# Kernel optimization log

Hardware: AMD Instinct MI355X
Metric: run time of the kernel (lower is better)

Reference implementation:

```python
import jax, jax.numpy as jnp
import numpy as np

D = 1024        # d_model
H = 16          # n_heads
DF = 4096       # d_ff
MAXL = 1024     # max_len
MAXSTEPS = 24   # max_steps


def setup_inputs() -> dict:
    key = jax.random.key(0)
    ks = jax.random.split(key, 10)
    B, S = 4, 1024
    s = 0.02
    f32 = jnp.float32
    return {
        "x": jax.random.normal(ks[0], (B, S, D), f32),
        "original_input": jax.random.normal(ks[1], (B, S, D), f32),
        "think_step": 5,
        "step_embed": jax.random.normal(ks[2], (MAXSTEPS, D), f32) * s,
        "Wqkv": jax.random.normal(ks[3], (D, 3 * D), f32) * s,
        "bqkv": jnp.zeros((3 * D,), f32),
        "Wout": jax.random.normal(ks[4], (D, D), f32) * s,
        "bout": jnp.zeros((D,), f32),
        "Wg": jax.random.normal(ks[5], (2 * D, D), f32) * s,
        "bg": jnp.zeros((D,), f32),
        "rel_pos_bias": jax.random.normal(ks[6], (2 * MAXL - 1,), f32) * s,
        "W1": jax.random.normal(ks[7], (D, DF), f32) * s,
        "b1": jnp.zeros((DF,), f32),
        "W2": jax.random.normal(ks[8], (DF, D), f32) * s,
        "b2": jnp.zeros((D,), f32),
        "ln1_g": jnp.ones((D,), f32),
        "ln1_b": jnp.zeros((D,), f32),
        "ln2_g": jnp.ones((D,), f32),
        "ln2_b": jnp.zeros((D,), f32),
    }


def _layer_norm(x, g, b, eps=1e-5):
    m = jnp.mean(x, axis=-1, keepdims=True)
    v = jnp.mean((x - m) ** 2, axis=-1, keepdims=True)
    return (x - m) * jax.lax.rsqrt(v + eps) * g + b


def reference(x, original_input, think_step, step_embed, Wqkv, bqkv, Wout, bout,
              Wg, bg, rel_pos_bias, W1, b1, W2, b2, ln1_g, ln1_b, ln2_g, ln2_b):
    B, S, _ = x.shape
    hd = D // H
    # gated residual input injection
    gate = jax.nn.sigmoid(jnp.concatenate([x, original_input], axis=-1) @ Wg + bg)
    x = x * (1.0 - gate) + original_input * gate
    # think-step embedding (clamped)
    step = min(int(think_step), MAXSTEPS - 1)
    x = x + step_embed[step][None, None, :]
    # qkv projection -> (3, B, H, S, hd)
    qkv = (x @ Wqkv + bqkv).reshape(B, S, 3, H, hd).transpose(2, 0, 3, 1, 4)
    q, k, v = qkv[0], qkv[1], qkv[2]
    scores = jnp.einsum('bhqd,bhkd->bhqk', q, k) * (hd ** -0.5)
    # relative position bias: dist clamped to [0, 2*MAXL-2]
    pos = jnp.arange(S)
    rel = jnp.clip(pos[:, None] - pos[None, :] + (MAXL - 1), 0, 2 * MAXL - 2)
    scores = scores + rel_pos_bias[rel][None, None]  # (B,H,S,S)
    probs = jax.nn.softmax(scores, axis=-1)
    attn = jnp.einsum('bhqk,bhkd->bhqd', probs, v)
    attn = attn.transpose(0, 2, 1, 3).reshape(B, S, D)
    attn = attn @ Wout + bout
    x = _layer_norm(x + attn, ln1_g, ln1_b)
    h = jax.nn.gelu(x @ W1 + b1, approximate=False) @ W2 + b2
    return _layer_norm(x + h, ln2_g, ln2_b)
```

## Files before the change

kernel.cpp:

```cpp
#include <hip/hip_runtime.h>
#include <hip/hip_bf16.h>
#include <math.h>

#define D_MODEL 1024
#define NH      16
#define HD      64
#define DFF     4096
#define SEQ     1024
#define BATCH   4
#define TOK     (BATCH*SEQ)
#define MAXSTEPS 24

typedef __hip_bfloat16 bf16;
typedef __attribute__((ext_vector_type(8))) short short8;
typedef __attribute__((ext_vector_type(4))) float floatx4;

__device__ __forceinline__ float b2f(bf16 v){ return __bfloat162float(v); }
__device__ __forceinline__ bf16  f2b(float v){ return __float2bfloat16(v); }

__device__ __forceinline__ void gload_lds16(const bf16* g, bf16* l){
    __builtin_amdgcn_global_load_lds((const __attribute__((address_space(1))) void*)g,
                                     (__attribute__((address_space(3))) void*)l, 16, 0, 0);
}

template<int TN, int EPI, bool SPLITK>
__global__ __launch_bounds__(256)
void mfma_gemm(const bf16* __restrict__ A, const bf16* __restrict__ Bt,
               const float* __restrict__ bias, void* __restrict__ outv,
               void* __restrict__ outv2,
               int M, int N, int K, int lda, int ldb,
               const float* __restrict__ xg, const float* __restrict__ og,
               const float* __restrict__ seg, const int* __restrict__ stepp)
{
    constexpr int NT  = TN / 32;
    constexpr int NBP = TN / 64;
    constexpr int R   = (TN == 64) ? 4 : 3;
    __shared__ bf16 As[R][128 * 32];
    __shared__ bf16 Bs[R][TN * 32];
    const int tid  = threadIdx.x;
    const int lane = tid & 63;
    const int w    = tid >> 6;
    const int wm   = w & 1, wn = w >> 1;
    const int fr   = lane & 15;
    const int q    = lane >> 4;

    if (SPLITK) {
        int z = blockIdx.z;
        A  += (size_t)z * K;
        Bt += (size_t)z * K;
    }

    const int tn_g = gridDim.x;
    const int nwg  = tn_g * gridDim.y;
    const int bid  = blockIdx.y * tn_g + blockIdx.x;
    const int o    = (bid & 7) * (nwg >> 3) + (bid >> 3);
    const int bandw = 8 * tn_g;
    const int band  = o / bandw;
    const int rr    = o - band * bandw;
    const int row0 = (band * 8 + (rr & 7)) * 128;
    const int col0 = (rr >> 3) * TN;

    const bf16* gA[2]; int sA_[2];
    #pragma unroll
    for (int p = 0; p < 2; ++p) {
        int s  = p * 256 + tid;
        int m  = s >> 2;
        int qg = (s & 3) ^ ((m >> 1) & 3);
        gA[p]  = A + (size_t)(row0 + m) * lda + qg * 8;
        sA_[p] = s * 8;
    }
    const bf16* gB[NBP]; int sB_[NBP];
    #pragma unroll
    for (int p = 0; p < NBP; ++p) {
        int s  = p * 256 + tid;
        int m  = s >> 2;
        int qg = (s & 3) ^ ((m >> 1) & 3);
        gB[p]  = Bt + (size_t)(col0 + m) * ldb + qg * 8;
        sB_[p] = s * 8;
    }

    int aoff[4], boff[NT];
    #pragma unroll
    for (int t = 0; t < 4; ++t) {
        int ml  = wm * 64 + t * 16 + fr;
        aoff[t] = (ml * 4 + (q ^ ((ml >> 1) & 3))) * 8;
    }
    #pragma unroll
    for (int t = 0; t < NT; ++t) {
        int nl  = wn * (TN / 2) + t * 16 + fr;
        boff[t] = (nl * 4 + (q ^ ((nl >> 1) & 3))) * 8;
    }

    #pragma unroll
    for (int pt = 0; pt < R - 1; ++pt) {
        #pragma unroll
        for (int p = 0; p < 2; ++p)   gload_lds16(gA[p] + pt * 32, &As[pt][sA_[p]]);
        #pragma unroll
        for (int p = 0; p < NBP; ++p) gload_lds16(gB[p] + pt * 32, &Bs[pt][sB_[p]]);
    }

    floatx4 acc[4][NT] = {};
    const int nk = K >> 5;
    int cur = 0;
    int kst = (R - 1) * 32;

    for (int t = 0; t < nk; ++t) {
        if constexpr (TN == 64) asm volatile("s_waitcnt vmcnt(6)" ::: "memory");
        else                    asm volatile("s_waitcnt vmcnt(4)" ::: "memory");
        __builtin_amdgcn_s_barrier();
        asm volatile("" ::: "memory");

        if (kst < K) {
            int sb = (cur == 0) ? (R - 1) : (cur - 1);
            #pragma unroll
            for (int p = 0; p < 2; ++p)   gload_lds16(gA[p] + kst, &As[sb][sA_[p]]);
            #pragma unroll
            for (int p = 0; p < NBP; ++p) gload_lds16(gB[p] + kst, &Bs[sb][sB_[p]]);
            kst += 32;
        }

        short8 af[4], bfg[NT];
        #pragma unroll
        for (int i = 0; i < 4; ++i)  af[i]  = *(const short8*)(&As[cur][aoff[i]]);
        #pragma unroll
        for (int j = 0; j < NT; ++j) bfg[j] = *(const short8*)(&Bs[cur][boff[j]]);
        #pragma unroll
        for (int i = 0; i < 4; ++i)
            #pragma unroll
            for (int j = 0; j < NT; ++j)
                acc[i][j] = __builtin_amdgcn_mfma_f32_16x16x32_bf16(af[i], bfg[j], acc[i][j], 0, 0, 0);

        cur = (cur == R - 1) ? 0 : (cur + 1);
    }

    void* outp = outv;
    float bscale = 1.0f;
    if (SPLITK && blockIdx.z != 0) { outp = outv2; bscale = 0.0f; }

    int st = 0;
    if (EPI == 3) {
        st = stepp[0];
        st = st < 0 ? 0 : (st > MAXSTEPS - 1 ? MAXSTEPS - 1 : st);
    }

    float bv[NT], sv[NT];
    #pragma unroll
    for (int nt = 0; nt < NT; ++nt) {
        int col = col0 + wn * (TN / 2) + nt * 16 + fr;
        bv[nt] = bias[col] * bscale;
        if (EPI == 3) sv[nt] = seg[st * D_MODEL + col];
    }
    #pragma unroll
    for (int mt = 0; mt < 4; ++mt) {
        #pragma unroll
        for (int nt = 0; nt < NT; ++nt) {
            int col = col0 + wn * (TN / 2) + nt * 16 + fr;
            #pragma unroll
            for (int r = 0; r < 4; ++r) {
                int row = row0 + wm * 64 + mt * 16 + q * 4 + r;
                float v = acc[mt][nt][r] + bv[nt];
                if (EPI == 0) {
                    ((float*)outp)[(size_t)row * N + col] = v;
                } else if (EPI == 1) {
                    ((bf16*)outp)[(size_t)row * N + col] = f2b(v);
                } else if (EPI == 2) {
                    float g = 0.5f * v * (1.0f + erff(v * 0.70710678118654752f));
                    ((bf16*)outp)[(size_t)row * N + col] = f2b(g);
                } else if (EPI == 3) {
                    float g = 1.0f / (1.0f + __expf(-v));
                    size_t idx = (size_t)row * N + col;
                    float mix = xg[idx] * (1.0f - g) + og[idx] * g + sv[nt];
                    ((bf16*)outp)[idx] = f2b(mix);
                } else {
                    if (col0 < 2048) {
                        ((bf16*)outp)[(size_t)row * N + col] = f2b(v);
                    } else {
                        int b = row >> 10, s = row & 1023;
                        int hh = (col - 2048) >> 6, d = (col - 2048) & 63;
                        ((bf16*)outv2)[((size_t)((b * NH + hh) * 64 + d)) * SEQ + s] = f2b(v);
                    }
                }
            }
        }
    }
}

__global__ __launch_bounds__(256, 2)
void gemm_wide_gelu(const bf16* __restrict__ A, const bf16* __restrict__ Bt,
                    const float* __restrict__ bias, bf16* __restrict__ out,
                    int M, int N, int K)
{
    constexpr int R = 3;
    __shared__ bf16 As[R][256 * 32];
    __shared__ bf16 Bs[R][128 * 32];
    const int tid  = threadIdx.x;
    const int lane = tid & 63;
    const int w    = tid >> 6;
    const int wm   = w & 1, wn = w >> 1;
    const int fr   = lane & 15;
    const int q    = lane >> 4;

    const int tn_g = gridDim.x;
    const int nwg  = tn_g * gridDim.y;
    const int bid  = blockIdx.y * tn_g + blockIdx.x;
    const int o    = (bid & 7) * (nwg >> 3) + (bid >> 3);
    const int bandw = 8 * tn_g;
    const int band  = o / bandw;
    const int rr    = o - band * bandw;
    const int row0 = (band * 8 + (rr & 7)) * 256;
    const int col0 = (rr >> 3) * 128;

    const bf16* gA[4]; int sA_[4];
    #pragma unroll
    for (int p = 0; p < 4; ++p) {
        int s  = p * 256 + tid;
        int m  = s >> 2;
        int qg = (s & 3) ^ ((m >> 1) & 3);
        gA[p]  = A + (size_t)(row0 + m) * K + qg * 8;
        sA_[p] = s * 8;
    }
    const bf16* gB[2]; int sB_[2];
    #pragma unroll
    for (int p = 0; p < 2; ++p) {
        int s  = p * 256 + tid;
        int m  = s >> 2;
        int qg = (s & 3) ^ ((m >> 1) & 3);
        gB[p]  = Bt + (size_t)(col0 + m) * K + qg * 8;
        sB_[p] = s * 8;
    }

    int aoff[8], boff[4];
    #pragma unroll
    for (int t = 0; t < 8; ++t) {
        int ml  = wm * 128 + t * 16 + fr;
        aoff[t] = (ml * 4 + (q ^ ((ml >> 1) & 3))) * 8;
    }
    #pragma unroll
    for (int t = 0; t < 4; ++t) {
        int nl  = wn * 64 + t * 16 + fr;
        boff[t] = (nl * 4 + (q ^ ((nl >> 1) & 3))) * 8;
    }

    #pragma unroll
    for (int pt = 0; pt < R - 1; ++pt) {
        #pragma unroll
        for (int p = 0; p < 4; ++p) gload_lds16(gA[p] + pt * 32, &As[pt][sA_[p]]);
        #pragma unroll
        for (int p = 0; p < 2; ++p) gload_lds16(gB[p] + pt * 32, &Bs[pt][sB_[p]]);
    }

    floatx4 acc[8][4] = {};
    const int nk = K >> 5;
    int cur = 0;
    int kst = (R - 1) * 32;

    for (int t = 0; t < nk; ++t) {
        asm volatile("s_waitcnt vmcnt(6)" ::: "memory");
        __builtin_amdgcn_s_barrier();
        asm volatile("" ::: "memory");

        if (kst < K) {
            int sb = (cur == 0) ? (R - 1) : (cur - 1);
            #pragma unroll
            for (int p = 0; p < 4; ++p) gload_lds16(gA[p] + kst, &As[sb][sA_[p]]);
            #pragma unroll
            for (int p = 0; p < 2; ++p) gload_lds16(gB[p] + kst, &Bs[sb][sB_[p]]);
            kst += 32;
        }

        short8 af[8], bfg[4];
        #pragma unroll
        for (int i = 0; i < 8; ++i) af[i]  = *(const short8*)(&As[cur][aoff[i]]);
        #pragma unroll
        for (int j = 0; j < 4; ++j) bfg[j] = *(const short8*)(&Bs[cur][boff[j]]);
        __builtin_amdgcn_s_setprio(1);
        #pragma unroll
        for (int i = 0; i < 8; ++i)
            #pragma unroll
            for (int j = 0; j < 4; ++j)
                acc[i][j] = __builtin_amdgcn_mfma_f32_16x16x32_bf16(af[i], bfg[j], acc[i][j], 0, 0, 0);
        __builtin_amdgcn_s_setprio(0);

        cur = (cur == R - 1) ? 0 : (cur + 1);
    }

    float bv[4];
    #pragma unroll
    for (int j = 0; j < 4; ++j) bv[j] = bias[col0 + wn * 64 + j * 16 + fr];
    #pragma unroll
    for (int mt = 0; mt < 8; ++mt) {
        #pragma unroll
        for (int nt = 0; nt < 4; ++nt) {
            int col = col0 + wn * 64 + nt * 16 + fr;
            #pragma unroll
            for (int r = 0; r < 4; ++r) {
                int row = row0 + wm * 128 + mt * 16 + q * 4 + r;
                float v = acc[mt][nt][r] + bv[nt];
                float g = 0.5f * v * (1.0f + erff(v * 0.70710678118654752f));
                out[(size_t)row * N + col] = f2b(g);
            }
        }
    }
}

#define NTRANS_BLOCKS 14336
__global__ __launch_bounds__(256)
void transpose_all_kernel(const float* __restrict__ Wg,   bf16* __restrict__ WgT,
                          const float* __restrict__ Wqkv, bf16* __restrict__ WqkvT,
                          const float* __restrict__ Wout, bf16* __restrict__ WoutT,
                          const float* __restrict__ W1,   bf16* __restrict__ W1T,
                          const float* __restrict__ W2,   bf16* __restrict__ W2T)
{
    __shared__ float t[32][33];
    const int bid = blockIdx.x;
    if (bid >= NTRANS_BLOCKS) return;
    const float* W; bf16* WT; int K, N, base;
    if      (bid <  2048) { W = Wg;   WT = WgT;   K = 2048; N = 1024; base = 0; }
    else if (bid <  5120) { W = Wqkv; WT = WqkvT; K = 1024; N = 3072; base = 2048; }
    else if (bid <  6144) { W = Wout; WT = WoutT; K = 1024; N = 1024; base = 5120; }
    else if (bid < 10240) { W = W1;   WT = W1T;   K = 1024; N = 4096; base = 6144; }
    else                  { W = W2;   WT = W2T;   K = 4096; N = 1024; base = 10240; }
    const int lb  = bid - base;
    const int ntx = N >> 5;
    const int n0 = (lb % ntx) * 32, k0 = (lb / ntx) * 32;
    const int tx = threadIdx.x & 31, ty = threadIdx.x >> 5;
    #pragma unroll
    for (int i = 0; i < 4; ++i)
        t[ty + i * 8][tx] = W[(size_t)(k0 + ty + i * 8) * N + n0 + tx];
    __syncthreads();
    #pragma unroll
    for (int i = 0; i < 4; ++i)
        WT[(size_t)(n0 + ty + i * 8) * K + k0 + tx] = f2b(t[tx][ty + i * 8]);
}

__global__ __launch_bounds__(256)
void xcat_kernel(const float* __restrict__ x, const float* __restrict__ orig,
                 bf16* __restrict__ xcat)
{
    int i = blockIdx.x * 256 + threadIdx.x;
    float4 xv = ((const float4*)x)[i];
    float4 ov = ((const float4*)orig)[i];
    int t = i >> 8, c4 = (i & 255) * 4;
    bf16* px = xcat + (size_t)t * 2048 + c4;
    px[0] = f2b(xv.x); px[1] = f2b(xv.y); px[2] = f2b(xv.z); px[3] = f2b(xv.w);
    bf16* po = px + 1024;
    po[0] = f2b(ov.x); po[1] = f2b(ov.y); po[2] = f2b(ov.z); po[3] = f2b(ov.w);
}

__global__ __launch_bounds__(256)
void fattn_kernel(const bf16* __restrict__ qkv, const bf16* __restrict__ Vt,
                  const float* __restrict__ relb, bf16* __restrict__ out)
{
    __shared__ bf16 KPs[128 * 64];
    __shared__ bf16 Vs [64 * 128];
    __shared__ float relb_s[1088];

    const int tid  = threadIdx.x;
    const int lane = tid & 63;
    const int w    = tid >> 6;
    const int fr   = lane & 15;
    const int quad = lane >> 4;

    const int qt = blockIdx.x & 15;
    const int h  = (blockIdx.x >> 4) & 15;
    const int b  = blockIdx.x >> 8;
    const int bq = b * SEQ;
    const int bh = b * NH + h;

    for (int i = tid; i < 1087; i += 256)
        relb_s[i] = relb[qt * 64 + i] - 8.0f;

    const int qrow = bq + qt * 64 + w * 16 + fr;
    short8 qf[2];
    {
        const bf16* qp = qkv + (size_t)qrow * 3072 + h * 64 + quad * 8;
        qf[0] = *(const short8*)(qp);
        qf[1] = *(const short8*)(qp + 32);
    }

    int ibase[4];
    #pragma unroll
    for (int r = 0; r < 4; ++r)
        ibase[r] = (w * 16 + quad * 4 + r) - fr + 1023;

    float lsum[4] = {0.f, 0.f, 0.f, 0.f};
    floatx4 accO[4];
    #pragma unroll
    for (int nt = 0; nt < 4; ++nt) accO[nt] = (floatx4){0.f, 0.f, 0.f, 0.f};

    for (int k0 = 0; k0 < SEQ; k0 += 128) {
        __syncthreads();
        #pragma unroll
        for (int it = 0; it < 4; ++it) {
            int s = it * 256 + tid;
            int key = s >> 3, cs = s & 7;
            int c = cs ^ (key & 7);
            const bf16* src = qkv + (size_t)(bq + k0 + key) * 3072 + 1024 + h * 64 + c * 8;
            gload_lds16(src, KPs + (size_t)s * 8);
        }
        #pragma unroll
        for (int it = 0; it < 4; ++it) {
            int s = it * 256 + tid;
            int row = s >> 4, cs = s & 15;
            int c = cs ^ (row & 15);
            const bf16* src = Vt + (size_t)(bh * 64 + row) * SEQ + k0 + c * 8;
            gload_lds16(src, Vs + (size_t)s * 8);
        }
        __syncthreads();

        floatx4 accS[8];
        #pragma unroll
        for (int t = 0; t < 8; ++t) accS[t] = (floatx4){0.f, 0.f, 0.f, 0.f};
        __builtin_amdgcn_s_setprio(1);
        #pragma unroll
        for (int t = 0; t < 8; ++t) {
            int row = t * 16 + fr;
            #pragma unroll
            for (int ks = 0; ks < 2; ++ks) {
                int slot = (ks * 4 + quad) ^ (row & 7);
                short8 kf = *(const short8*)(KPs + (size_t)row * 64 + slot * 8);
                accS[t] = __builtin_amdgcn_mfma_f32_16x16x32_bf16(qf[ks], kf, accS[t], 0, 0, 0);
            }
        }
        __builtin_amdgcn_s_setprio(0);

        __syncthreads();

        bf16* Ps = KPs + w * 2048;
        #pragma unroll
        for (int t = 0; t < 8; ++t) {
            int keyl = t * 16 + fr;
            int cbase = keyl >> 3, koff = keyl & 7;
            #pragma unroll
            for (int r = 0; r < 4; ++r) {
                float bias = relb_s[ibase[r] - k0 - t * 16];
                float p = __expf(fmaf(accS[t][r], 0.125f, bias));
                lsum[r] += p;
                int row = quad * 4 + r;
                int slot = cbase ^ (row & 15);
                Ps[(size_t)row * 128 + slot * 8 + koff] = f2b(p);
            }
        }

        __builtin_amdgcn_s_setprio(1);
        #pragma unroll
        for (int ks = 0; ks < 4; ++ks) {
            int slotp = (ks * 4 + quad) ^ (fr & 15);
            short8 pf = *(const short8*)(Ps + (size_t)fr * 128 + slotp * 8);
            #pragma unroll
            for (int nt = 0; nt < 4; ++nt) {
                int vrow = nt * 16 + fr;
                int slotv = (ks * 4 + quad) ^ (vrow & 15);
                short8 vf = *(const short8*)(Vs + (size_t)vrow * 128 + slotv * 8);
                accO[nt] = __builtin_amdgcn_mfma_f32_16x16x32_bf16(pf, vf, accO[nt], 0, 0, 0);
            }
        }
        __builtin_amdgcn_s_setprio(0);
    }

    float inv[4];
    #pragma unroll
    for (int r = 0; r < 4; ++r) {
        float v = lsum[r];
        v += __shfl_xor(v, 1); v += __shfl_xor(v, 2);
        v += __shfl_xor(v, 4); v += __shfl_xor(v, 8);
        inv[r] = 1.0f / v;
    }

    #pragma unroll
    for (int nt = 0; nt < 4; ++nt) {
        int col = h * 64 + nt * 16 + fr;
        #pragma unroll
        for (int r = 0; r < 4; ++r) {
            int t = bq + qt * 64 + w * 16 + quad * 4 + r;
            out[(size_t)t * D_MODEL + col] = f2b(accO[nt][r] * inv[r]);
        }
    }
}

template<bool OUT_BF16, bool HAS2>
__global__ __launch_bounds__(256)
void ln_kernel(const bf16* __restrict__ a, const float* __restrict__ add,
               const float* __restrict__ add2,
               const float* __restrict__ g, const float* __restrict__ bb,
               void* __restrict__ outv)
{
    __shared__ float red[256];
    __shared__ float red2[256];
    const int row = blockIdx.x;
    const int tid = threadIdx.x;
    float s[4];
    float lsum = 0.f, lsq = 0.f;
    #pragma unroll
    for (int u = 0; u < 4; ++u) {
        int i = tid + 256 * u;
        float v = b2f(a[row * D_MODEL + i]) + add[row * D_MODEL + i];
        if (HAS2) v += add2[row * D_MODEL + i];
        s[u] = v; lsum += v; lsq += v * v;
    }
    red[tid] = lsum; red2[tid] = lsq; __syncthreads();
    for (int s2 = 128; s2 > 0; s2 >>= 1) {
        if (tid < s2) { red[tid] += red[tid + s2]; red2[tid] += red2[tid + s2]; }
        __syncthreads();
    }
    float mean = red[0] * (1.0f / D_MODEL);
    float var  = red2[0] * (1.0f / D_MODEL) - mean * mean;
    float rs = rsqrtf(var + 1e-5f);
    #pragma unroll
    for (int u = 0; u < 4; ++u) {
        int i = tid + 256 * u;
        float o = (s[u] - mean) * rs * g[i] + bb[i];
        if (OUT_BF16) ((bf16*)outv)[row * D_MODEL + i] = f2b(o);
        else          ((float*)outv)[row * D_MODEL + i] = o;
    }
}

extern "C" void kernel_launch(void* const* d_in, const int* in_sizes, int n_in,
                              void* d_out, int out_size, void* d_ws, size_t ws_size,
                              hipStream_t stream)
{
    const float* x     = (const float*)d_in[0];
    const float* orig  = (const float*)d_in[1];
    const int*   step  = (const int*)  d_in[2];
    const float* se    = (const float*)d_in[3];
    const float* Wqkv  = (const float*)d_in[4];
    const float* bqkv  = (const float*)d_in[5];
    const float* Wout  = (const float*)d_in[6];
    const float* bout  = (const float*)d_in[7];
    const float* Wg    = (const float*)d_in[8];
    const float* bg    = (const float*)d_in[9];
    const float* relb  = (const float*)d_in[10];
    const float* W1    = (const float*)d_in[11];
    const float* b1    = (const float*)d_in[12];
    const float* W2    = (const float*)d_in[13];
    const float* b2    = (const float*)d_in[14];
    const float* ln1g  = (const float*)d_in[15];
    const float* ln1b  = (const float*)d_in[16];
    const float* ln2g  = (const float*)d_in[17];
    const float* ln2b  = (const float*)d_in[18];

    char* ws = (char*)d_ws;
    bf16* WgT   = (bf16*)(ws);
    bf16* WqkvT = (bf16*)(ws + ( 4u << 20));
    bf16* WoutT = (bf16*)(ws + (10u << 20));
    bf16* W1T   = (bf16*)(ws + (12u << 20));
    bf16* W2T   = (bf16*)(ws + (20u << 20));
    bf16* xw    = (bf16*)(ws + (28u << 20));
    bf16* xcat  = (bf16*)(ws + (36u << 20));
    bf16* attnb = (bf16*)(ws + (36u << 20));
    bf16* h     = (bf16*)(ws + (44u << 20));
    bf16* qkvb  = (bf16*)(ws + (52u << 20));
    float* tmp2 = (float*)(ws);
    bf16* Vt    = (bf16*)d_out;
    float* tmp  = (float*)d_out;

    dim3 blk(256);

    transpose_all_kernel<<<NTRANS_BLOCKS, blk, 0, stream>>>(Wg, WgT, Wqkv, WqkvT,
                                                    Wout, WoutT, W1, W1T, W2, W2T);
    xcat_kernel<<<TOK, blk, 0, stream>>>(x, orig, xcat);

    mfma_gemm<64, 3, false><<<dim3(D_MODEL/64, TOK/128), blk, 0, stream>>>(
        xcat, WgT, bg, xw, nullptr, TOK, D_MODEL, 2*D_MODEL, 2*D_MODEL, 2*D_MODEL,
        x, orig, se, step);

    mfma_gemm<128, 4, false><<<dim3(3*D_MODEL/128, TOK/128), blk, 0, stream>>>(
        xw, WqkvT, bqkv, qkvb, Vt, TOK, 3*D_MODEL, D_MODEL, D_MODEL, D_MODEL,
        nullptr, nullptr, nullptr, nullptr);

    fattn_kernel<<<BATCH*NH*(SEQ/64), blk, 0, stream>>>(qkvb, Vt, relb, attnb);

    mfma_gemm<64, 0, false><<<dim3(D_MODEL/64, TOK/128), blk, 0, stream>>>(
        attnb, WoutT, bout, tmp, nullptr, TOK, D_MODEL, D_MODEL, D_MODEL, D_MODEL,
        nullptr, nullptr, nullptr, nullptr);

    ln_kernel<true, false><<<TOK, blk, 0, stream>>>(xw, tmp, nullptr, ln1g, ln1b, xw);

    gemm_wide_gelu<<<dim3(DFF/128, TOK/256), blk, 0, stream>>>(
        xw, W1T, b1, h, TOK, DFF, D_MODEL);

    mfma_gemm<128, 0, true><<<dim3(D_MODEL/128, TOK/128, 2), blk, 0, stream>>>(
        h, W2T, b2, tmp, tmp2, TOK, D_MODEL, DFF/2, DFF, DFF,
        nullptr, nullptr, nullptr, nullptr);

    ln_kernel<false, true><<<TOK, blk, 0, stream>>>(xw, tmp, tmp2, ln2g, ln2b, d_out);
}
```

Baseline: 429.5 us.

## Fuse fp32-to-bf16 cast into gate GEMM, use wide GEMM for QKV

Adds a gate GEMM that reads x and original_input in fp32 directly, converts them to bf16 while staging into LDS, and runs the sigmoid-mix epilogue, so the separate concat/cast kernel and its buffer are gone. The QKV projection moves to the 256-row wide GEMM template with a plain bf16 epilogue. A separate transpose kernel then builds the V layout for attention, where the old scattered transposed-store epilogue used to do it. The gate GEMM trades async LDS loads of A for register-staged conversion with only double buffering, and the extra transpose adds a launch plus another pass over V.

```diff
diff --git a/kernel.cpp b/kernel.cpp
--- a/kernel.cpp
+++ b/kernel.cpp
@@ -28,9 +28,7 @@
 void mfma_gemm(const bf16* __restrict__ A, const bf16* __restrict__ Bt,
                const float* __restrict__ bias, void* __restrict__ outv,
                void* __restrict__ outv2,
-               int M, int N, int K, int lda, int ldb,
-               const float* __restrict__ xg, const float* __restrict__ og,
-               const float* __restrict__ seg, const int* __restrict__ stepp)
+               int M, int N, int K, int lda, int ldb)
 {
     constexpr int NT  = TN / 32;
     constexpr int NBP = TN / 64;
@@ -137,19 +135,10 @@
     float bscale = 1.0f;
     if (SPLITK && blockIdx.z != 0) { outp = outv2; bscale = 0.0f; }
 
-    int st = 0;
-    if (EPI == 3) {
-        st = stepp[0];
-        st = st < 0 ? 0 : (st > MAXSTEPS - 1 ? MAXSTEPS - 1 : st);
-    }
-
-    float bv[NT], sv[NT];
-    #pragma unroll
-    for (int nt = 0; nt < NT; ++nt) {
-        int col = col0 + wn * (TN / 2) + nt * 16 + fr;
-        bv[nt] = bias[col] * bscale;
-        if (EPI == 3) sv[nt] = seg[st * D_MODEL + col];
-    }
+    float bv[NT];
+    #pragma unroll
+    for (int nt = 0; nt < NT; ++nt)
+        bv[nt] = bias[col0 + wn * (TN / 2) + nt * 16 + fr] * bscale;
     #pragma unroll
     for (int mt = 0; mt < 4; ++mt) {
         #pragma unroll
@@ -159,36 +148,18 @@
             for (int r = 0; r < 4; ++r) {
                 int row = row0 + wm * 64 + mt * 16 + q * 4 + r;
                 float v = acc[mt][nt][r] + bv[nt];
-                if (EPI == 0) {
-                    ((float*)outp)[(size_t)row * N + col] = v;
-                } else if (EPI == 1) {
-                    ((bf16*)outp)[(size_t)row * N + col] = f2b(v);
-                } else if (EPI == 2) {
-                    float g = 0.5f * v * (1.0f + erff(v * 0.70710678118654752f));
-                    ((bf16*)outp)[(size_t)row * N + col] = f2b(g);
-                } else if (EPI == 3) {
-                    float g = 1.0f / (1.0f + __expf(-v));
-                    size_t idx = (size_t)row * N + col;
-                    float mix = xg[idx] * (1.0f - g) + og[idx] * g + sv[nt];
-                    ((bf16*)outp)[idx] = f2b(mix);
-                } else {
-                    if (col0 < 2048) {
-                        ((bf16*)outp)[(size_t)row * N + col] = f2b(v);
-                    } else {
-                        int b = row >> 10, s = row & 1023;
-                        int hh = (col - 2048) >> 6, d = (col - 2048) & 63;
-                        ((bf16*)outv2)[((size_t)((b * NH + hh) * 64 + d)) * SEQ + s] = f2b(v);
-                    }
-                }
+                if (EPI == 0) ((float*)outp)[(size_t)row * N + col] = v;
+                else          ((bf16*)outp)[(size_t)row * N + col] = f2b(v);
             }
         }
     }
 }
 
+template<int EPI>
 __global__ __launch_bounds__(256, 2)
-void gemm_wide_gelu(const bf16* __restrict__ A, const bf16* __restrict__ Bt,
-                    const float* __restrict__ bias, bf16* __restrict__ out,
-                    int M, int N, int K)
+void gemm_wide(const bf16* __restrict__ A, const bf16* __restrict__ Bt,
+               const float* __restrict__ bias, bf16* __restrict__ out,
+               int M, int N, int K)
 {
     constexpr int R = 3;
     __shared__ bf16 As[R][256 * 32];
@@ -296,8 +267,135 @@
             for (int r = 0; r < 4; ++r) {
                 int row = row0 + wm * 128 + mt * 16 + q * 4 + r;
                 float v = acc[mt][nt][r] + bv[nt];
-                float g = 0.5f * v * (1.0f + erff(v * 0.70710678118654752f));
-                out[(size_t)row * N + col] = f2b(g);
+                if (EPI == 1) {
+                    out[(size_t)row * N + col] = f2b(v);
+                } else {
+                    float g = 0.5f * v * (1.0f + erff(v * 0.70710678118654752f));
+                    out[(size_t)row * N + col] = f2b(g);
+                }
+            }
+        }
+    }
+}
+
+__global__ __launch_bounds__(256)
+void gemm_gate(const float* __restrict__ x, const float* __restrict__ orig,
+               const bf16* __restrict__ Bt, const float* __restrict__ bias,
+               bf16* __restrict__ out, const float* __restrict__ se,
+               const int* __restrict__ stepp)
+{
+    __shared__ bf16 As[2][128 * 32];
+    __shared__ bf16 Bs[2][64 * 32];
+    const int tid  = threadIdx.x;
+    const int lane = tid & 63;
+    const int w    = tid >> 6;
+    const int wm   = w & 1, wn = w >> 1;
+    const int fr   = lane & 15;
+    const int q    = lane >> 4;
+
+    const int tn_g = gridDim.x;
+    const int nwg  = tn_g * gridDim.y;
+    const int bid  = blockIdx.y * tn_g + blockIdx.x;
+    const int o    = (bid & 7) * (nwg >> 3) + (bid >> 3);
+    const int bandw = 8 * tn_g;
+    const int band  = o / bandw;
+    const int rr    = o - band * bandw;
+    const int row0 = (band * 8 + (rr & 7)) * 128;
+    const int col0 = (rr >> 3) * 64;
+
+    int sA_[2], mrow[2], colA[2];
+    #pragma unroll
+    for (int p = 0; p < 2; ++p) {
+        int s   = p * 256 + tid;
+        int m   = s >> 2;
+        int qg  = (s & 3) ^ ((m >> 1) & 3);
+        mrow[p] = m; colA[p] = qg * 8; sA_[p] = s * 8;
+    }
+    const bf16* gB; int sB_;
+    {
+        int m  = tid >> 2;
+        int qg = (tid & 3) ^ ((m >> 1) & 3);
+        gB  = Bt + (size_t)(col0 + m) * 2048 + qg * 8;
+        sB_ = tid * 8;
+    }
+
+    int aoff[4], boff[2];
+    #pragma unroll
+    for (int t = 0; t < 4; ++t) {
+        int ml  = wm * 64 + t * 16 + fr;
+        aoff[t] = (ml * 4 + (q ^ ((ml >> 1) & 3))) * 8;
+    }
+    #pragma unroll
+    for (int t = 0; t < 2; ++t) {
+        int nl  = wn * 32 + t * 16 + fr;
+        boff[t] = (nl * 4 + (q ^ ((nl >> 1) & 3))) * 8;
+    }
+
+#define STAGE_A(BUF, K0)                                                      \
+    { _Pragma("unroll")                                                       \
+      for (int p = 0; p < 2; ++p) {                                           \
+          int col = (K0) + colA[p];                                           \
+          const float* src = (col < 1024)                                     \
+              ? (x    + (size_t)(row0 + mrow[p]) * 1024 + col)                \
+              : (orig + (size_t)(row0 + mrow[p]) * 1024 + (col - 1024));      \
+          float4 a0 = *(const float4*)src;                                    \
+          float4 a1 = *(const float4*)(src + 4);                              \
+          bf16 tb[8];                                                         \
+          tb[0]=f2b(a0.x); tb[1]=f2b(a0.y); tb[2]=f2b(a0.z); tb[3]=f2b(a0.w); \
+          tb[4]=f2b(a1.x); tb[5]=f2b(a1.y); tb[6]=f2b(a1.z); tb[7]=f2b(a1.w); \
+          *(short8*)(&As[BUF][sA_[p]]) = *(const short8*)tb;                  \
+      } }
+
+    STAGE_A(0, 0);
+    gload_lds16(gB, &Bs[0][sB_]);
+
+    floatx4 acc[4][2] = {};
+    __syncthreads();
+
+    int cur = 0;
+    for (int k0 = 32; k0 <= 2048; k0 += 32) {
+        if (k0 < 2048) {
+            STAGE_A(cur ^ 1, k0);
+            gload_lds16(gB + k0, &Bs[cur ^ 1][sB_]);
+        }
+        short8 af[4], bfg[2];
+        #pragma unroll
+        for (int i = 0; i < 4; ++i) af[i]  = *(const short8*)(&As[cur][aoff[i]]);
+        #pragma unroll
+        for (int j = 0; j < 2; ++j) bfg[j] = *(const short8*)(&Bs[cur][boff[j]]);
+        #pragma unroll
+        for (int i = 0; i < 4; ++i)
+            #pragma unroll
+            for (int j = 0; j < 2; ++j)
+                acc[i][j] = __builtin_amdgcn_mfma_f32_16x16x32_bf16(af[i], bfg[j], acc[i][j], 0, 0, 0);
+        __syncthreads();
+        cur ^= 1;
+    }
+#undef STAGE_A
+
+    int st = stepp[0];
+    st = st < 0 ? 0 : (st > MAXSTEPS - 1 ? MAXSTEPS - 1 : st);
+
+    float bv[2], sv[2];
+    #pragma unroll
+    for (int nt = 0; nt < 2; ++nt) {
+        int col = col0 + wn * 32 + nt * 16 + fr;
+        bv[nt] = bias[col];
+        sv[nt] = se[st * D_MODEL + col];
+    }
+    #pragma unroll
+    for (int mt = 0; mt < 4; ++mt) {
+        #pragma unroll
+        for (int nt = 0; nt < 2; ++nt) {
+            int col = col0 + wn * 32 + nt * 16 + fr;
+            #pragma unroll
+            for (int r = 0; r < 4; ++r) {
+                int row = row0 + wm * 64 + mt * 16 + q * 4 + r;
+                float v = acc[mt][nt][r] + bv[nt];
+                float g = 1.0f / (1.0f + __expf(-v));
+                size_t idx = (size_t)row * D_MODEL + col;
+                float mix = x[idx] * (1.0f - g) + orig[idx] * g + sv[nt];
+                out[idx] = f2b(mix);
             }
         }
     }
@@ -334,17 +432,24 @@
 }
 
 __global__ __launch_bounds__(256)
-void xcat_kernel(const float* __restrict__ x, const float* __restrict__ orig,
-                 bf16* __restrict__ xcat)
-{
-    int i = blockIdx.x * 256 + threadIdx.x;
-    float4 xv = ((const float4*)x)[i];
-    float4 ov = ((const float4*)orig)[i];
-    int t = i >> 8, c4 = (i & 255) * 4;
-    bf16* px = xcat + (size_t)t * 2048 + c4;
-    px[0] = f2b(xv.x); px[1] = f2b(xv.y); px[2] = f2b(xv.z); px[3] = f2b(xv.w);
-    bf16* po = px + 1024;
-    po[0] = f2b(ov.x); po[1] = f2b(ov.y); po[2] = f2b(ov.z); po[3] = f2b(ov.w);
+void vtrans_kernel(const bf16* __restrict__ qkv, bf16* __restrict__ Vt)
+{
+    __shared__ float t[32][33];
+    const int blk = blockIdx.x;
+    const int dt = blk & 1;
+    const int st = (blk >> 1) & 31;
+    const int h  = (blk >> 6) & 15;
+    const int b  = blk >> 10;
+    const int tx = threadIdx.x & 31, ty = threadIdx.x >> 5;
+    #pragma unroll
+    for (int i = 0; i < 4; ++i)
+        t[ty + i * 8][tx] = b2f(qkv[(size_t)(b * SEQ + st * 32 + ty + i * 8) * 3072
+                                    + 2048 + h * 64 + dt * 32 + tx]);
+    __syncthreads();
+    #pragma unroll
+    for (int i = 0; i < 4; ++i)
+        Vt[(size_t)((b * NH + h) * 64 + dt * 32 + ty + i * 8) * SEQ + st * 32 + tx]
+            = f2b(t[tx][ty + i * 8]);
 }
 
 __global__ __launch_bounds__(256)
@@ -546,7 +651,6 @@
     bf16* W1T   = (bf16*)(ws + (12u << 20));
     bf16* W2T   = (bf16*)(ws + (20u << 20));
     bf16* xw    = (bf16*)(ws + (28u << 20));
-    bf16* xcat  = (bf16*)(ws + (36u << 20));
     bf16* attnb = (bf16*)(ws + (36u << 20));
     bf16* h     = (bf16*)(ws + (44u << 20));
     bf16* qkvb  = (bf16*)(ws + (52u << 20));
@@ -558,30 +662,27 @@
 
     transpose_all_kernel<<<NTRANS_BLOCKS, blk, 0, stream>>>(Wg, WgT, Wqkv, WqkvT,
                                                     Wout, WoutT, W1, W1T, W2, W2T);
-    xcat_kernel<<<TOK, blk, 0, stream>>>(x, orig, xcat);
-
-    mfma_gemm<64, 3, false><<<dim3(D_MODEL/64, TOK/128), blk, 0, stream>>>(
-        xcat, WgT, bg, xw, nullptr, TOK, D_MODEL, 2*D_MODEL, 2*D_MODEL, 2*D_MODEL,
-        x, orig, se, step);
-
-    mfma_gemm<128, 4, false><<<dim3(3*D_MODEL/128, TOK/128), blk, 0, stream>>>(
-        xw, WqkvT, bqkv, qkvb, Vt, TOK, 3*D_MODEL, D_MODEL, D_MODEL, D_MODEL,
-        nullptr, nullptr, nullptr, nullptr);
+
+    gemm_gate<<<dim3(D_MODEL/64, TOK/128), blk, 0, stream>>>(
+        x, orig, WgT, bg, xw, se, step);
+
+    gemm_wide<1><<<dim3(3*D_MODEL/128, TOK/256), blk, 0, stream>>>(
+        xw, WqkvT, bqkv, qkvb, TOK, 3*D_MODEL, D_MODEL);
+
+    vtrans_kernel<<<BATCH*NH*64, blk, 0, stream>>>(qkvb, Vt);
 
     fattn_kernel<<<BATCH*NH*(SEQ/64), blk, 0, stream>>>(qkvb, Vt, relb, attnb);
 
     mfma_gemm<64, 0, false><<<dim3(D_MODEL/64, TOK/128), blk, 0, stream>>>(
-        attnb, WoutT, bout, tmp, nullptr, TOK, D_MODEL, D_MODEL, D_MODEL, D_MODEL,
-        nullptr, nullptr, nullptr, nullptr);
+        attnb, WoutT, bout, tmp, nullptr, TOK, D_MODEL, D_MODEL, D_MODEL, D_MODEL);
 
     ln_kernel<true, false><<<TOK, blk, 0, stream>>>(xw, tmp, nullptr, ln1g, ln1b, xw);
 
-    gemm_wide_gelu<<<dim3(DFF/128, TOK/256), blk, 0, stream>>>(
+    gemm_wide<2><<<dim3(DFF/128, TOK/256), blk, 0, stream>>>(
         xw, W1T, b1, h, TOK, DFF, D_MODEL);
 
     mfma_gemm<128, 0, true><<<dim3(D_MODEL/128, TOK/128, 2), blk, 0, stream>>>(
-        h, W2T, b2, tmp, tmp2, TOK, D_MODEL, DFF/2, DFF, DFF,
-        nullptr, nullptr, nullptr, nullptr);
+        h, W2T, b2, tmp, tmp2, TOK, D_MODEL, DFF/2, DFF, DFF);
 
     ln_kernel<false, true><<<TOK, blk, 0, stream>>>(xw, tmp, tmp2, ln2g, ln2b, d_out);
 }
```

Result: slower. 456.9 us (+6.4%).
